# Kernel tuning notes

Measured on AMD Instinct MI355X. Metric: run time of the kernel, lower is better.

Reference implementation:

```python
import jax, jax.numpy as jnp
import numpy as np

EMB = 768
HEADS = 8

def setup_inputs() -> dict:
    key = jax.random.key(0)
    ks = jax.random.split(key, 5)
    x = jax.random.normal(ks[0], (8, 2048, EMB), dtype=jnp.float32)
    s = 1.0 / np.sqrt(EMB)
    W_qkv = jax.random.normal(ks[1], (EMB, 3 * EMB), dtype=jnp.float32) * s
    b_qkv = jnp.zeros((3 * EMB,), dtype=jnp.float32)
    W_proj = jax.random.normal(ks[2], (EMB, EMB), dtype=jnp.float32) * s
    b_proj = jnp.zeros((EMB,), dtype=jnp.float32)
    return {"x": x, "W_qkv": W_qkv, "b_qkv": b_qkv, "W_proj": W_proj, "b_proj": b_proj}

def reference(x, W_qkv, b_qkv, W_proj, b_proj):
    B, N, E = x.shape
    H = HEADS
    D = E // H
    qkv = x @ W_qkv + b_qkv  # [B, N, 3E]
    q, k, v = jnp.split(qkv, 3, axis=-1)
    # [B, N, E] -> [B, H, N, D]
    def heads(t):
        return t.reshape(B, N, H, D).transpose(0, 2, 1, 3)
    q, k, v = heads(q), heads(k), heads(v)
    # NOTE: original scales by 1/sqrt(emb_size), not 1/sqrt(head_dim)
    dots = jnp.einsum('bhnd,bhmd->bhnm', q, k) / jnp.sqrt(jnp.float32(E))
    attn = jax.nn.softmax(dots, axis=-1)  # dropout inactive (eval mode)
    out = jnp.einsum('bhnm,bhmd->bhnd', attn, v)
    out = out.transpose(0, 2, 1, 3).reshape(B, N, E)
    return out @ W_proj + b_proj
```

## Files before the change

### kernel.cpp

```cpp
#include <hip/hip_runtime.h>
#include <hip/hip_bf16.h>

typedef __attribute__((ext_vector_type(8))) short bf16x8;
typedef __attribute__((ext_vector_type(4))) short bf16x4;
typedef __attribute__((ext_vector_type(4))) float f32x4;
typedef __attribute__((ext_vector_type(16))) float f32x16;
typedef __attribute__((ext_vector_type(4))) unsigned int uint4v;

__device__ __forceinline__ short f2bf(float f) {
    unsigned int u = __float_as_uint(f);
    u += 0x7FFFu + ((u >> 16) & 1u);
    return (short)(u >> 16);
}

__device__ __forceinline__ unsigned cvtpk(float lo, float hi) {
    unsigned r;
    asm("v_cvt_pk_bf16_f32 %0, %1, %2" : "=v"(r) : "v"(lo), "v"(hi));
    return r;
}

__global__ __launch_bounds__(256) void cast_kernel(const float* __restrict__ in,
                                                   short* __restrict__ out, int n4) {
    int i = blockIdx.x * 256 + threadIdx.x;
    if (i >= n4) return;
    const f32x4 v = *(const f32x4*)(in + (size_t)i * 4);
    bf16x4 o;
    o[0] = f2bf(v[0]); o[1] = f2bf(v[1]); o[2] = f2bf(v[2]); o[3] = f2bf(v[3]);
    *(bf16x4*)(out + (size_t)i * 4) = o;
}

__global__ __launch_bounds__(256) void transpose_cast_kernel(const float* __restrict__ W,
                                                             short* __restrict__ WT,
                                                             int R, int C) {
    __shared__ float tile[64][65];
    const int bc = blockIdx.x * 64;
    const int br = blockIdx.y * 64;
    const int t = threadIdx.x;
#pragma unroll
    for (int i = 0; i < 16; ++i) {
        int o = t + 256 * i;
        int r = o >> 6, c = o & 63;
        tile[r][c] = W[(size_t)(br + r) * C + bc + c];
    }
    __syncthreads();
#pragma unroll
    for (int i = 0; i < 16; ++i) {
        int o = t + 256 * i;
        int c = o >> 6, r = o & 63;
        WT[(size_t)(bc + c) * R + br + r] = f2bf(tile[r][c]);
    }
}

#define GPAD 72
__global__ __launch_bounds__(256, 2) void gemm1_kernel(
    const short* __restrict__ A, const short* __restrict__ BT,
    const float* __restrict__ bias,
    short* __restrict__ Qh, short* __restrict__ Kh, short* __restrict__ Vt)
{
    __shared__ short As[128][GPAD];
    __shared__ short Bs[128][GPAD];
    const int K = 768;
    const int t = threadIdx.x;
    const int w = t >> 6, l = t & 63;
    const int wr = w >> 1, wc = w & 1;
    const int lr = l & 15, lg = l >> 4;

    const size_t Abase = (size_t)blockIdx.x * 128 * K;
    const size_t Bbase = (size_t)blockIdx.y * 128 * K;

    const f32x4 z4 = {0.f, 0.f, 0.f, 0.f};
    f32x4 acc[4][4];
#pragma unroll
    for (int i = 0; i < 4; ++i)
#pragma unroll
        for (int j = 0; j < 4; ++j) acc[i][j] = z4;

    for (int kt = 0; kt < K; kt += 64) {
#pragma unroll
        for (int i = 0; i < 4; ++i) {
            int o = t + 256 * i;
            int r = o >> 3, kc = o & 7;
            *(bf16x8*)&As[r][kc * 8] = *(const bf16x8*)(A + Abase + (size_t)r * K + kt + kc * 8);
            *(bf16x8*)&Bs[r][kc * 8] = *(const bf16x8*)(BT + Bbase + (size_t)r * K + kt + kc * 8);
        }
        __syncthreads();
#pragma unroll
        for (int kk = 0; kk < 2; ++kk) {
            bf16x8 af[4], bfr[4];
#pragma unroll
            for (int mi = 0; mi < 4; ++mi)
                af[mi] = *(const bf16x8*)&As[wr * 64 + mi * 16 + lr][kk * 32 + lg * 8];
#pragma unroll
            for (int ni = 0; ni < 4; ++ni)
                bfr[ni] = *(const bf16x8*)&Bs[wc * 64 + ni * 16 + lr][kk * 32 + lg * 8];
#pragma unroll
            for (int mi = 0; mi < 4; ++mi)
#pragma unroll
                for (int ni = 0; ni < 4; ++ni)
                    acc[mi][ni] = __builtin_amdgcn_mfma_f32_16x16x32_bf16(
                        af[mi], bfr[ni], acc[mi][ni], 0, 0, 0);
        }
        __syncthreads();
    }

    const int rb = blockIdx.x * 128 + wr * 64;
    const int cb = blockIdx.y * 128 + wc * 64;
#pragma unroll
    for (int ni = 0; ni < 4; ++ni) {
        const int c = cb + ni * 16 + lr;
        const float bv = bias[c];
        const int which = (c >= 1536) ? 2 : (c >= 768 ? 1 : 0);
        const int cc = c - which * 768;
        const int h = cc / 96;
        const int d = cc - h * 96;
#pragma unroll
        for (int mi = 0; mi < 4; ++mi) {
            const int r0 = rb + mi * 16 + lg * 4;
            const int b = r0 >> 11, n0 = r0 & 2047;
            const int hb = b * 8 + h;
            if (which == 2) {
                bf16x4 pk;
#pragma unroll
                for (int r = 0; r < 4; ++r) pk[r] = f2bf(acc[mi][ni][r] + bv);
                *(bf16x4*)&Vt[((size_t)hb * 96 + d) * 2048 + n0] = pk;
            } else {
                short* dst = which ? Kh : Qh;
#pragma unroll
                for (int r = 0; r < 4; ++r)
                    dst[((size_t)hb * 2048 + n0 + r) * 96 + d] = f2bf(acc[mi][ni][r] + bv);
            }
        }
    }
}

__global__ __launch_bounds__(256, 2) void attn_kernel(
    const short* __restrict__ Qh, const short* __restrict__ Kh,
    const short* __restrict__ Vt, short* __restrict__ AO)
{
    __shared__ __align__(16) char smem[27136];
    short (*Qs)[104] = (short (*)[104])smem;
    short (*Ks)[104] = (short (*)[104])smem;
    short (*Vs)[72]  = (short (*)[72])(smem + 13312);
    __shared__ float ltab[4][32];

    const int t = threadIdx.x;
    const int w = t >> 6, l = t & 63;
    const int ql = l & 31, hi = l >> 5;
    const float scale = 0.03608439182435161f;

    const unsigned L = blockIdx.y * 16 + blockIdx.x;
    const int bh = (int)((L & 7) * 8 + ((L >> 3) & 7));
    const int qt = (int)(L >> 6);

    const short* Qg = Qh + (size_t)bh * 2048 * 96 + (size_t)qt * 128 * 96;
    const short* Kg = Kh + (size_t)bh * 2048 * 96;
    const short* Vg = Vt + (size_t)bh * 96 * 2048;

#pragma unroll
    for (int i = 0; i < 6; ++i) {
        int o = t + 256 * i;
        *(bf16x8*)&Qs[o / 12][(o % 12) * 8] = *(const bf16x8*)(Qg + 8 * (size_t)o);
    }
    __syncthreads();

    bf16x8 kreg[3], vreg[3];
#pragma unroll
    for (int i = 0; i < 3; ++i) {
        int o = t + 256 * i;
        kreg[i] = *(const bf16x8*)(Kg + 8 * (size_t)o);
        vreg[i] = *(const bf16x8*)(Vg + (size_t)(o >> 3) * 2048 + (o & 7) * 8);
    }

    bf16x8 qf[6];
#pragma unroll
    for (int kk = 0; kk < 6; ++kk)
        qf[kk] = *(const bf16x8*)&Qs[w * 32 + ql][kk * 16 + hi * 8];
    __syncthreads();

    f32x16 oacc[3];
#pragma unroll
    for (int i = 0; i < 3; ++i)
#pragma unroll
        for (int r = 0; r < 16; ++r) oacc[i][r] = 0.f;
    float lacc = 0.f;

    for (int kt = 0; kt < 32; ++kt) {
#pragma unroll
        for (int i = 0; i < 3; ++i) {
            int o = t + 256 * i;
            *(bf16x8*)&Ks[o / 12][(o % 12) * 8] = kreg[i];
            *(bf16x8*)&Vs[o >> 3][(o & 7) * 8] = vreg[i];
        }
        __syncthreads();

        if (kt != 31) {
            const size_t koff = (size_t)(kt + 1) * 64 * 96;
            const int moff = (kt + 1) * 64;
#pragma unroll
            for (int i = 0; i < 3; ++i) {
                int o = t + 256 * i;
                kreg[i] = *(const bf16x8*)(Kg + koff + 8 * (size_t)o);
                vreg[i] = *(const bf16x8*)(Vg + (size_t)(o >> 3) * 2048 + moff + (o & 7) * 8);
            }
        }

        f32x16 sa0, sa1;
#pragma unroll
        for (int r = 0; r < 16; ++r) { sa0[r] = 0.f; sa1[r] = 0.f; }
#pragma unroll
        for (int kk = 0; kk < 6; ++kk) {
            bf16x8 kf0 = *(const bf16x8*)&Ks[ql][kk * 16 + hi * 8];
            bf16x8 kf1 = *(const bf16x8*)&Ks[32 + ql][kk * 16 + hi * 8];
            sa0 = __builtin_amdgcn_mfma_f32_32x32x16_bf16(kf0, qf[kk], sa0, 0, 0, 0);
            sa1 = __builtin_amdgcn_mfma_f32_32x32x16_bf16(kf1, qf[kk], sa1, 0, 0, 0);
        }

        bf16x8 pa[4];
#pragma unroll
        for (int mi = 0; mi < 2; ++mi) {
            float p[16];
#pragma unroll
            for (int r = 0; r < 16; ++r) {
                float s = (mi == 0 ? sa0[r] : sa1[r]) * scale;
                p[r] = __expf(s);
                lacc += p[r];
            }
            unsigned x0 = cvtpk(p[0], p[1]),  y0 = cvtpk(p[4], p[5]);
            unsigned x1 = cvtpk(p[2], p[3]),  y1 = cvtpk(p[6], p[7]);
            unsigned x2 = cvtpk(p[8], p[9]),  y2 = cvtpk(p[12], p[13]);
            unsigned x3 = cvtpk(p[10], p[11]), y3 = cvtpk(p[14], p[15]);
            asm("v_permlane32_swap_b32 %0, %1" : "+v"(x0), "+v"(y0));
            asm("v_permlane32_swap_b32 %0, %1" : "+v"(x1), "+v"(y1));
            asm("v_permlane32_swap_b32 %0, %1" : "+v"(x2), "+v"(y2));
            asm("v_permlane32_swap_b32 %0, %1" : "+v"(x3), "+v"(y3));
            uint4v uA; uA[0] = x0; uA[1] = x1; uA[2] = y0; uA[3] = y1;
            uint4v uB; uB[0] = x2; uB[1] = x3; uB[2] = y2; uB[3] = y3;
            pa[mi * 2 + 0] = __builtin_bit_cast(bf16x8, uA);
            pa[mi * 2 + 1] = __builtin_bit_cast(bf16x8, uB);
        }

#pragma unroll
        for (int kb = 0; kb < 4; ++kb) {
#pragma unroll
            for (int db = 0; db < 3; ++db) {
                bf16x8 vf = *(const bf16x8*)&Vs[db * 32 + ql][kb * 16 + hi * 8];
                oacc[db] = __builtin_amdgcn_mfma_f32_32x32x16_bf16(pa[kb], vf, oacc[db], 0, 0, 0);
            }
        }
        __syncthreads();
    }

    float lsum = lacc + __shfl_xor(lacc, 32);
    if (l < 32) ltab[w][l] = lsum;
    asm volatile("s_waitcnt lgkmcnt(0)" ::: "memory");

    float linv[16];
#pragma unroll
    for (int r = 0; r < 16; ++r) {
        const int q = (r & 3) + 8 * (r >> 2) + 4 * hi;
        linv[r] = 1.0f / ltab[w][q];
    }

    const int b = bh >> 3, h = bh & 7;
    const size_t rowbase = (size_t)b * 2048 + qt * 128 + w * 32;
#pragma unroll
    for (int db = 0; db < 3; ++db) {
#pragma unroll
        for (int r = 0; r < 16; ++r) {
            const int q = (r & 3) + 8 * (r >> 2) + 4 * hi;
            AO[(rowbase + q) * 768 + h * 96 + db * 32 + ql] = f2bf(oacc[db][r] * linv[r]);
        }
    }
}

__global__ __launch_bounds__(256, 2) void gemm2_kernel(
    const short* __restrict__ A, const short* __restrict__ BT,
    const float* __restrict__ bias, float* __restrict__ out)
{
    __shared__ short As[128][GPAD];
    __shared__ short Bs[128][GPAD];
    const int K = 768;
    const int t = threadIdx.x;
    const int w = t >> 6, l = t & 63;
    const int wr = w >> 1, wc = w & 1;
    const int lr = l & 15, lg = l >> 4;

    const size_t Abase = (size_t)blockIdx.x * 128 * K;
    const size_t Bbase = (size_t)blockIdx.y * 128 * K;

    const f32x4 z4 = {0.f, 0.f, 0.f, 0.f};
    f32x4 acc[4][4];
#pragma unroll
    for (int i = 0; i < 4; ++i)
#pragma unroll
        for (int j = 0; j < 4; ++j) acc[i][j] = z4;

    for (int kt = 0; kt < K; kt += 64) {
#pragma unroll
        for (int i = 0; i < 4; ++i) {
            int o = t + 256 * i;
            int r = o >> 3, kc = o & 7;
            *(bf16x8*)&As[r][kc * 8] = *(const bf16x8*)(A + Abase + (size_t)r * K + kt + kc * 8);
            *(bf16x8*)&Bs[r][kc * 8] = *(const bf16x8*)(BT + Bbase + (size_t)r * K + kt + kc * 8);
        }
        __syncthreads();
#pragma unroll
        for (int kk = 0; kk < 2; ++kk) {
            bf16x8 af[4], bfr[4];
#pragma unroll
            for (int mi = 0; mi < 4; ++mi)
                af[mi] = *(const bf16x8*)&As[wr * 64 + mi * 16 + lr][kk * 32 + lg * 8];
#pragma unroll
            for (int ni = 0; ni < 4; ++ni)
                bfr[ni] = *(const bf16x8*)&Bs[wc * 64 + ni * 16 + lr][kk * 32 + lg * 8];
#pragma unroll
            for (int mi = 0; mi < 4; ++mi)
#pragma unroll
                for (int ni = 0; ni < 4; ++ni)
                    acc[mi][ni] = __builtin_amdgcn_mfma_f32_16x16x32_bf16(
                        af[mi], bfr[ni], acc[mi][ni], 0, 0, 0);
        }
        __syncthreads();
    }

    const int rb = blockIdx.x * 128 + wr * 64;
    const int cb = blockIdx.y * 128 + wc * 64;
#pragma unroll
    for (int ni = 0; ni < 4; ++ni) {
        const int c = cb + ni * 16 + lr;
        const float bv = bias[c];
#pragma unroll
        for (int mi = 0; mi < 4; ++mi) {
            const int r0 = rb + mi * 16 + lg * 4;
#pragma unroll
            for (int r = 0; r < 4; ++r)
                out[(size_t)(r0 + r) * 768 + c] = acc[mi][ni][r] + bv;
        }
    }
}

extern "C" void kernel_launch(void* const* d_in, const int* in_sizes, int n_in,
                              void* d_out, int out_size, void* d_ws, size_t ws_size,
                              hipStream_t stream) {
    const float* x     = (const float*)d_in[0];
    const float* Wqkv  = (const float*)d_in[1];
    const float* bqkv  = (const float*)d_in[2];
    const float* Wproj = (const float*)d_in[3];
    const float* bproj = (const float*)d_in[4];
    float* out = (float*)d_out;

    char* ws = (char*)d_ws;
    short* xb     = (short*)(ws);
    short* WqkvT  = (short*)(ws + 25165824);
    short* WprojT = (short*)(ws + 28704768);
    short* Qh     = (short*)(ws + 29884416);
    short* Kh     = (short*)(ws + 55050240);
    short* Vt     = (short*)(ws + 80216064);
    short* AO     = xb;

    cast_kernel<<<12288, 256, 0, stream>>>(x, xb, 3145728);
    transpose_cast_kernel<<<dim3(36, 12), 256, 0, stream>>>(Wqkv, WqkvT, 768, 2304);
    transpose_cast_kernel<<<dim3(12, 12), 256, 0, stream>>>(Wproj, WprojT, 768, 768);
    gemm1_kernel<<<dim3(128, 18), 256, 0, stream>>>(xb, WqkvT, bqkv, Qh, Kh, Vt);
    attn_kernel<<<dim3(16, 64), 256, 0, stream>>>(Qh, Kh, Vt, AO);
    gemm2_kernel<<<dim3(128, 6), 256, 0, stream>>>(AO, WprojT, bproj, out);
}
```

Before: 255.0 us.

## Double-buffer K/V tiles in LDS, prescale Q for exp2, remap block order

The attention kernel now ping-pongs between two LDS buffers for K and V and prefetches two tiles ahead, which cuts the synchronisations per key tile from two to one. The softmax scale and log2(e) are folded into Q when the QKV GEMM writes it out, so exp becomes a bare exp2 with no multiply. The block-to-(batch·head, q-tile) mapping is changed so that neighbouring blocks share a head's K/V, and s_setprio is raised around the MFMA sections. LDS use doubles to about 54 KB, which may limit occupancy, and quantising the prescaled Q to bf16 changes rounding slightly.

After: 237.5 us. 1.07x faster.

```diff
diff --git a/kernel.cpp b/kernel.cpp
--- a/kernel.cpp
+++ b/kernel.cpp
@@ -103,6 +103,7 @@
         __syncthreads();
     }
 
+    const float qs = 0.05205877f;
     const int rb = blockIdx.x * 128 + wr * 64;
     const int cb = blockIdx.y * 128 + wc * 64;
 #pragma unroll
@@ -123,11 +124,14 @@
 #pragma unroll
                 for (int r = 0; r < 4; ++r) pk[r] = f2bf(acc[mi][ni][r] + bv);
                 *(bf16x4*)&Vt[((size_t)hb * 96 + d) * 2048 + n0] = pk;
+            } else if (which == 1) {
+#pragma unroll
+                for (int r = 0; r < 4; ++r)
+                    Kh[((size_t)hb * 2048 + n0 + r) * 96 + d] = f2bf(acc[mi][ni][r] + bv);
             } else {
-                short* dst = which ? Kh : Qh;
 #pragma unroll
                 for (int r = 0; r < 4; ++r)
-                    dst[((size_t)hb * 2048 + n0 + r) * 96 + d] = f2bf(acc[mi][ni][r] + bv);
+                    Qh[((size_t)hb * 2048 + n0 + r) * 96 + d] = f2bf((acc[mi][ni][r] + bv) * qs);
             }
         }
     }
@@ -137,32 +141,26 @@
     const short* __restrict__ Qh, const short* __restrict__ Kh,
     const short* __restrict__ Vt, short* __restrict__ AO)
 {
-    __shared__ __align__(16) char smem[27136];
-    short (*Qs)[104] = (short (*)[104])smem;
-    short (*Ks)[104] = (short (*)[104])smem;
-    short (*Vs)[72]  = (short (*)[72])(smem + 13312);
+    __shared__ __align__(16) char smem[54272];
+    short (*Ks0)[104] = (short (*)[104])smem;
+    short (*Ks1)[104] = (short (*)[104])(smem + 13312);
+    short (*Vs0)[72]  = (short (*)[72])(smem + 26624);
+    short (*Vs1)[72]  = (short (*)[72])(smem + 40448);
+    short (*Qs)[104]  = (short (*)[104])smem;
     __shared__ float ltab[4][32];
 
     const int t = threadIdx.x;
     const int w = t >> 6, l = t & 63;
     const int ql = l & 31, hi = l >> 5;
-    const float scale = 0.03608439182435161f;
 
     const unsigned L = blockIdx.y * 16 + blockIdx.x;
-    const int bh = (int)((L & 7) * 8 + ((L >> 3) & 7));
-    const int qt = (int)(L >> 6);
+    const int bh = (int)((L & 7) + 8 * (L >> 7));
+    const int qt = (int)((L >> 3) & 15);
 
     const short* Qg = Qh + (size_t)bh * 2048 * 96 + (size_t)qt * 128 * 96;
     const short* Kg = Kh + (size_t)bh * 2048 * 96;
     const short* Vg = Vt + (size_t)bh * 96 * 2048;
 
-#pragma unroll
-    for (int i = 0; i < 6; ++i) {
-        int o = t + 256 * i;
-        *(bf16x8*)&Qs[o / 12][(o % 12) * 8] = *(const bf16x8*)(Qg + 8 * (size_t)o);
-    }
-    __syncthreads();
-
     bf16x8 kreg[3], vreg[3];
 #pragma unroll
     for (int i = 0; i < 3; ++i) {
@@ -171,12 +169,32 @@
         vreg[i] = *(const bf16x8*)(Vg + (size_t)(o >> 3) * 2048 + (o & 7) * 8);
     }
 
+#pragma unroll
+    for (int i = 0; i < 6; ++i) {
+        int o = t + 256 * i;
+        *(bf16x8*)&Qs[o / 12][(o % 12) * 8] = *(const bf16x8*)(Qg + 8 * (size_t)o);
+    }
+    __syncthreads();
     bf16x8 qf[6];
 #pragma unroll
     for (int kk = 0; kk < 6; ++kk)
         qf[kk] = *(const bf16x8*)&Qs[w * 32 + ql][kk * 16 + hi * 8];
     __syncthreads();
 
+#pragma unroll
+    for (int i = 0; i < 3; ++i) {
+        int o = t + 256 * i;
+        *(bf16x8*)&Ks0[o / 12][(o % 12) * 8] = kreg[i];
+        *(bf16x8*)&Vs0[o >> 3][(o & 7) * 8] = vreg[i];
+    }
+#pragma unroll
+    for (int i = 0; i < 3; ++i) {
+        int o = t + 256 * i;
+        kreg[i] = *(const bf16x8*)(Kg + (size_t)64 * 96 + 8 * (size_t)o);
+        vreg[i] = *(const bf16x8*)(Vg + (size_t)(o >> 3) * 2048 + 64 + (o & 7) * 8);
+    }
+    __syncthreads();
+
     f32x16 oacc[3];
 #pragma unroll
     for (int i = 0; i < 3; ++i)
@@ -184,18 +202,19 @@
         for (int r = 0; r < 16; ++r) oacc[i][r] = 0.f;
     float lacc = 0.f;
 
-    for (int kt = 0; kt < 32; ++kt) {
-#pragma unroll
-        for (int i = 0; i < 3; ++i) {
-            int o = t + 256 * i;
-            *(bf16x8*)&Ks[o / 12][(o % 12) * 8] = kreg[i];
-            *(bf16x8*)&Vs[o >> 3][(o & 7) * 8] = vreg[i];
-        }
-        __syncthreads();
-
-        if (kt != 31) {
-            const size_t koff = (size_t)(kt + 1) * 64 * 96;
-            const int moff = (kt + 1) * 64;
+    auto iter = [&](int kt, short (*rK)[104], short (*rV)[72],
+                    short (*wK)[104], short (*wV)[72]) {
+        if (kt < 31) {
+#pragma unroll
+            for (int i = 0; i < 3; ++i) {
+                int o = t + 256 * i;
+                *(bf16x8*)&wK[o / 12][(o % 12) * 8] = kreg[i];
+                *(bf16x8*)&wV[o >> 3][(o & 7) * 8] = vreg[i];
+            }
+        }
+        if (kt < 30) {
+            const size_t koff = (size_t)(kt + 2) * 64 * 96;
+            const int moff = (kt + 2) * 64;
 #pragma unroll
             for (int i = 0; i < 3; ++i) {
                 int o = t + 256 * i;
@@ -207,13 +226,15 @@
         f32x16 sa0, sa1;
 #pragma unroll
         for (int r = 0; r < 16; ++r) { sa0[r] = 0.f; sa1[r] = 0.f; }
+        __builtin_amdgcn_s_setprio(1);
 #pragma unroll
         for (int kk = 0; kk < 6; ++kk) {
-            bf16x8 kf0 = *(const bf16x8*)&Ks[ql][kk * 16 + hi * 8];
-            bf16x8 kf1 = *(const bf16x8*)&Ks[32 + ql][kk * 16 + hi * 8];
+            bf16x8 kf0 = *(const bf16x8*)&rK[ql][kk * 16 + hi * 8];
+            bf16x8 kf1 = *(const bf16x8*)&rK[32 + ql][kk * 16 + hi * 8];
             sa0 = __builtin_amdgcn_mfma_f32_32x32x16_bf16(kf0, qf[kk], sa0, 0, 0, 0);
             sa1 = __builtin_amdgcn_mfma_f32_32x32x16_bf16(kf1, qf[kk], sa1, 0, 0, 0);
         }
+        __builtin_amdgcn_s_setprio(0);
 
         bf16x8 pa[4];
 #pragma unroll
@@ -221,8 +242,7 @@
             float p[16];
 #pragma unroll
             for (int r = 0; r < 16; ++r) {
-                float s = (mi == 0 ? sa0[r] : sa1[r]) * scale;
-                p[r] = __expf(s);
+                p[r] = __builtin_amdgcn_exp2f(mi == 0 ? sa0[r] : sa1[r]);
                 lacc += p[r];
             }
             unsigned x0 = cvtpk(p[0], p[1]),  y0 = cvtpk(p[4], p[5]);
@@ -239,15 +259,22 @@
             pa[mi * 2 + 1] = __builtin_bit_cast(bf16x8, uB);
         }
 
+        __builtin_amdgcn_s_setprio(1);
 #pragma unroll
         for (int kb = 0; kb < 4; ++kb) {
 #pragma unroll
             for (int db = 0; db < 3; ++db) {
-                bf16x8 vf = *(const bf16x8*)&Vs[db * 32 + ql][kb * 16 + hi * 8];
+                bf16x8 vf = *(const bf16x8*)&rV[db * 32 + ql][kb * 16 + hi * 8];
                 oacc[db] = __builtin_amdgcn_mfma_f32_32x32x16_bf16(pa[kb], vf, oacc[db], 0, 0, 0);
             }
         }
-        __syncthreads();
+        __builtin_amdgcn_s_setprio(0);
+        __syncthreads();
+    };
+
+    for (int kt = 0; kt < 32; kt += 2) {
+        iter(kt,     Ks0, Vs0, Ks1, Vs1);
+        iter(kt + 1, Ks1, Vs1, Ks0, Vs0);
     }
 
     float lsum = lacc + __shfl_xor(lacc, 32);
```
